# Optimization experiments

Measured on AMD Instinct MI355X. Metric: run time of the kernel, lower is better.

Reference implementation:

```python
import jax, jax.numpy as jnp
import numpy as np

K = 1  # top-k experts per image


def cv_squared(v):
    # squared coefficient of variation; torch .var() is unbiased -> ddof=1
    eps = 1e-10
    m = v.mean()
    var = v.var(ddof=1)
    return jnp.where(jnp.abs(m) < eps, jnp.zeros((), v.dtype), var / (m * m + eps))


def setup_inputs() -> dict:
    key = jax.random.key(0)
    k0, k1, k2, k3 = jax.random.split(key, 4)
    B, H, W, C, E, HID = 64, 32, 32, 512, 5, 2048
    x = jax.random.normal(k0, (B, H, W, C), jnp.float32)
    # xavier-uniform-like scale for the gate
    gate_scale = float(np.sqrt(6.0 / (C + E)))
    w_gate = jax.random.uniform(k1, (C, E), jnp.float32, -gate_scale, gate_scale)
    W1 = jax.random.normal(k2, (E, C, HID), jnp.float32) * 0.02
    b1 = jnp.zeros((E, HID), jnp.float32)
    W2 = jax.random.normal(k3, (E, HID, C), jnp.float32) * 0.02
    b2 = jnp.zeros((E, C), jnp.float32)
    return {"x": x, "w_gate": w_gate, "W1": W1, "b1": b1, "W2": W2, "b2": b2}


def reference(x, w_gate, W1, b1, W2, b2):
    B, H, W_, C = x.shape
    E = w_gate.shape[1]
    xt = x.reshape(B, H * W_, C)              # [B, T, C] tokens
    xg = x.mean(axis=(1, 2))                  # [B, C] per-image gating feature

    # eval-mode noisy_top_k_gating (no noise): clean logits, clamp, top-k softmax
    logits = jnp.clip(xg @ w_gate, -50.0, 50.0)          # [B, E]
    top_logits, top_idx = jax.lax.top_k(logits, min(K + 1, E))
    tk_logits = top_logits[:, :K]
    tk_idx = top_idx[:, :K]                               # [B, K]
    tk_gates = jax.nn.softmax(tk_logits, axis=1)          # [B, K]
    gates = jnp.zeros_like(logits).at[jnp.arange(B)[:, None], tk_idx].set(tk_gates)

    importance = gates.sum(axis=0)                        # [E]
    load = (gates > 0).sum(axis=0).astype(jnp.float32)    # [E]
    loss = jnp.clip(cv_squared(importance) + cv_squared(load), 0.0, 1000.0)

    # dispatch: every token of image b goes through its top-K experts
    y = jnp.zeros_like(xt)
    for ki in range(K):
        idx = tk_idx[:, ki]                               # [B] expert id per image
        h = jnp.einsum('btd,bdh->bth', xt, W1[idx]) + b1[idx][:, None, :]
        h = jax.nn.gelu(h, approximate=False)             # torch nn.GELU default (erf)
        o = jnp.einsum('bth,bhd->btd', h, W2[idx]) + b2[idx][:, None, :]
        y = y + tk_gates[:, ki][:, None, None] * o

    return y.reshape(B, H, W_, C), loss
```

## Files before the change

### kernel.cpp

```cpp
#include <hip/hip_runtime.h>
#include <hip/hip_bf16.h>
#include <math.h>

typedef __attribute__((ext_vector_type(4))) float f4_t;
typedef __attribute__((ext_vector_type(8))) short s8_t;

constexpr int Bc = 64;
constexpr int Tc = 1024;
constexpr int Cc = 512;
constexpr int Ec = 5;
constexpr int HIDc = 2048;

__device__ __forceinline__ void async_copy16(const void* gsrc, void* ldst) {
  __builtin_amdgcn_global_load_lds(
      (const __attribute__((address_space(1))) unsigned int*)gsrc,
      (__attribute__((address_space(3))) unsigned int*)ldst, 16, 0, 0);
}

__device__ __forceinline__ float gelu_f(float v) {
  float u = v * 0.70710678118654752f;
  float ax = fabsf(u);
  float t = __frcp_rn(1.0f + 0.3275911f * ax);
  float p = t * (0.254829592f +
           t * (-0.284496736f +
           t * (1.421413741f +
           t * (-1.453152027f +
           t * 1.061405429f))));
  float er = 1.0f - p * __expf(-u * u);
  er = copysignf(er, u);
  return 0.5f * v * (1.0f + er);
}


__global__ void k_prep(const float* __restrict__ x, ushort* __restrict__ xbf,
                       float* __restrict__ part) {
  int b = blockIdx.x, p = blockIdx.y, tid = threadIdx.x;
  const float4* xp = (const float4*)(x + ((size_t)b * Tc + (size_t)p * 128) * Cc);
  ushort4* op = (ushort4*)(xbf + ((size_t)b * Tc + (size_t)p * 128) * Cc);
  int c4 = tid & 127, r0 = tid >> 7;
  float4 s = {0.f, 0.f, 0.f, 0.f};
  for (int r = r0; r < 128; r += 2) {
    float4 v = xp[(size_t)r * 128 + c4];
    s.x += v.x; s.y += v.y; s.z += v.z; s.w += v.w;
    union { __hip_bfloat16 h[4]; ushort4 u; } cv;
    cv.h[0] = __float2bfloat16(v.x);
    cv.h[1] = __float2bfloat16(v.y);
    cv.h[2] = __float2bfloat16(v.z);
    cv.h[3] = __float2bfloat16(v.w);
    op[(size_t)r * 128 + c4] = cv.u;
  }
  __shared__ float4 sh[128];
  if (r0) sh[c4] = s;
  __syncthreads();
  if (!r0) {
    float4 o = sh[c4];
    s.x += o.x; s.y += o.y; s.z += o.z; s.w += o.w;
    ((float4*)part)[(size_t)(b * 8 + p) * 128 + c4] = s;
  }
}

__global__ void k_partial(const float* __restrict__ x, float* __restrict__ part) {
  int b = blockIdx.x, p = blockIdx.y, tid = threadIdx.x;
  const float* xp = x + ((size_t)b * Tc + (size_t)p * 128) * Cc;
  float s0 = 0.f, s1 = 0.f;
  for (int t = 0; t < 128; ++t) {
    s0 += xp[(size_t)t * Cc + tid];
    s1 += xp[(size_t)t * Cc + tid + 256];
  }
  part[(size_t)(b * 8 + p) * Cc + tid] = s0;
  part[(size_t)(b * 8 + p) * Cc + tid + 256] = s1;
}

__global__ void k_cvt_x(const float* __restrict__ src, ushort* __restrict__ dst, int n4) {
  int i = blockIdx.x * blockDim.x + threadIdx.x;
  int stride = gridDim.x * blockDim.x;
  const float4* s4 = (const float4*)src;
  ushort4* d4 = (ushort4*)dst;
  for (; i < n4; i += stride) {
    float4 v = s4[i];
    union { __hip_bfloat16 h[4]; ushort4 u; } cv;
    cv.h[0] = __float2bfloat16(v.x);
    cv.h[1] = __float2bfloat16(v.y);
    cv.h[2] = __float2bfloat16(v.z);
    cv.h[3] = __float2bfloat16(v.w);
    d4[i] = cv.u;
  }
}

__global__ void k_xg_logits(const float* __restrict__ part, const float* __restrict__ wg,
                            float* __restrict__ logits) {
  __shared__ float xg[Cc];
  __shared__ float red[Ec][4];
  int b = blockIdx.x, tid = threadIdx.x;
  for (int c = tid; c < Cc; c += 256) {
    float s = 0.f;
#pragma unroll
    for (int p = 0; p < 8; ++p) s += part[(size_t)(b * 8 + p) * Cc + c];
    xg[c] = s * (1.0f / 1024.0f);
  }
  __syncthreads();
  float le[Ec] = {0.f, 0.f, 0.f, 0.f, 0.f};
  for (int c = tid; c < Cc; c += 256) {
    float v = xg[c];
#pragma unroll
    for (int e = 0; e < Ec; ++e) le[e] += v * wg[c * Ec + e];
  }
#pragma unroll
  for (int e = 0; e < Ec; ++e) {
    float v = le[e];
#pragma unroll
    for (int off = 32; off > 0; off >>= 1) v += __shfl_down(v, off);
    if ((tid & 63) == 0) red[e][tid >> 6] = v;
  }
  __syncthreads();
  if (tid < Ec) {
    float v = red[tid][0] + red[tid][1] + red[tid][2] + red[tid][3];
    v = fminf(fmaxf(v, -50.f), 50.f);
    logits[b * Ec + tid] = v;
  }
}

__global__ void k_gate(const float* __restrict__ logits, int* __restrict__ idx,
                       float* __restrict__ loss_out) {
  __shared__ int cnt[Ec];
  int tid = threadIdx.x;
  if (tid < Ec) cnt[tid] = 0;
  __syncthreads();
  if (tid < Bc) {
    const float* lb = logits + tid * Ec;
    int best = 0;
    float bv = lb[0];
#pragma unroll
    for (int e = 1; e < Ec; ++e) {
      float v = lb[e];
      if (v > bv) { bv = v; best = e; }
    }
    idx[tid] = best;
    atomicAdd(&cnt[best], 1);
  }
  __syncthreads();
  if (tid == 0) {
    const float mean = (float)Bc / (float)Ec;
    float var = 0.f;
#pragma unroll
    for (int e = 0; e < Ec; ++e) {
      float d = (float)cnt[e] - mean;
      var += d * d;
    }
    var *= (1.0f / (Ec - 1));
    float loss = 2.f * (var / (mean * mean + 1e-10f));
    loss = fminf(fmaxf(loss, 0.f), 1000.f);
    *loss_out = loss;
  }
}

__global__ void k_transpose_cvt(const float* __restrict__ src, __hip_bfloat16* __restrict__ dst,
                                int K, int N) {
  __shared__ float tile[32][33];
  int e = blockIdx.z;
  int kb = blockIdx.y * 32, nb = blockIdx.x * 32;
  const float* s = src + (size_t)e * K * N;
  __hip_bfloat16* d = dst + (size_t)e * K * N;
  int lx = threadIdx.x & 31, ly = threadIdx.x >> 5;
#pragma unroll
  for (int r = 0; r < 4; ++r) {
    int k = kb + ly + r * 8;
    tile[ly + r * 8][lx] = s[(size_t)k * N + nb + lx];
  }
  __syncthreads();
#pragma unroll
  for (int r = 0; r < 4; ++r) {
    int n = nb + ly + r * 8;
    d[(size_t)n * K + kb + lx] = __float2bfloat16(tile[lx][ly + r * 8]);
  }
}


__global__ __launch_bounds__(256, 2) void k_gemm1(
    const __hip_bfloat16* __restrict__ xbf, const __hip_bfloat16* __restrict__ w1t,
    const float* __restrict__ b1, const int* __restrict__ idx, int b0, int nz,
    __hip_bfloat16* __restrict__ h) {
  constexpr int K = Cc;
  constexpr int N = HIDc;
  constexpr int NT = K / 64;
  constexpr int NBX = N / 128, NBY = Tc / 128;
  __shared__ short lds[2][2][128 * 64];

  int nwg = NBX * NBY * nz;
  int cpx = nwg >> 3;
  int lg = (blockIdx.x & 7) * cpx + (blockIdx.x >> 3);
  int bx = lg % NBX, by = (lg / NBX) % NBY, bz = lg / (NBX * NBY);

  int e = idx[b0 + bz];
  int m0 = by * 128, n0 = bx * 128;
  const short* Ab = (const short*)xbf + ((size_t)bz * Tc + m0) * K;
  const short* Bb = (const short*)w1t + ((size_t)e * N + n0) * K;
  int tid = threadIdx.x, l = tid & 63, w = tid >> 6;
  int wr = w >> 1, wc = w & 1;

  const short* gA[4];
  const short* gB[4];
  int loff[4];
#pragma unroll
  for (int i = 0; i < 4; ++i) {
    int sp = i * 256 + tid;
    int r = sp >> 3;
    int c8 = ((sp & 7) ^ (r & 7)) << 3;
    gA[i] = Ab + (size_t)r * K + c8;
    gB[i] = Bb + (size_t)r * K + c8;
    loff[i] = sp * 16;
  }

  int arow = wr * 64 + (l & 15);
  int brow = wc * 64 + (l & 15);
  int s0 = (((l >> 4)) ^ (l & 7)) << 4;
  int s1 = (((l >> 4) + 4) ^ (l & 7)) << 4;

  f4_t acc[4][4] = {};

#pragma unroll
  for (int i = 0; i < 4; ++i) {
    async_copy16(gA[i], (char*)&lds[0][0][0] + loff[i]);
    async_copy16(gB[i], (char*)&lds[0][1][0] + loff[i]);
  }
  __syncthreads();

  for (int t = 0; t < NT; ++t) {
    int cur = t & 1;
    if (t + 1 < NT) {
      int k0 = (t + 1) * 64;
#pragma unroll
      for (int i = 0; i < 4; ++i) {
        async_copy16(gA[i] + k0, (char*)&lds[cur ^ 1][0][0] + loff[i]);
        async_copy16(gB[i] + k0, (char*)&lds[cur ^ 1][1][0] + loff[i]);
      }
    }
    const char* As = (const char*)&lds[cur][0][0];
    const char* Bs = (const char*)&lds[cur][1][0];
#pragma unroll
    for (int kk = 0; kk < 2; ++kk) {
      int sk = kk ? s1 : s0;
      s8_t a[4], b[4];
#pragma unroll
      for (int f = 0; f < 4; ++f) a[f] = *(const s8_t*)(As + (arow + f * 16) * 128 + sk);
#pragma unroll
      for (int f = 0; f < 4; ++f) b[f] = *(const s8_t*)(Bs + (brow + f * 16) * 128 + sk);
#pragma unroll
      for (int fm = 0; fm < 4; ++fm)
#pragma unroll
        for (int fn = 0; fn < 4; ++fn)
          acc[fm][fn] = __builtin_amdgcn_mfma_f32_16x16x32_bf16(a[fm], b[fn], acc[fm][fn], 0, 0, 0);
    }
    __syncthreads();
  }

  short* chunk = &lds[0][0][0] + w * (64 * 80);
  const float* bias = b1 + (size_t)e * N;
#pragma unroll
  for (int fn = 0; fn < 4; ++fn) {
    float bv = bias[n0 + wc * 64 + fn * 16 + (l & 15)];
#pragma unroll
    for (int fm = 0; fm < 4; ++fm) {
      int r4 = fm * 16 + ((l >> 4) << 2);
#pragma unroll
      for (int j = 0; j < 4; ++j) {
        float v = gelu_f(acc[fm][fn][j] + bv);
        chunk[(r4 + j) * 80 + fn * 16 + (l & 15)] =
            (short)__bfloat16_as_ushort(__float2bfloat16(v));
      }
    }
  }
  short* hb = (short*)(h + (size_t)bz * Tc * N);
  int cc = (l & 7) * 8;
#pragma unroll
  for (int p = 0; p < 8; ++p) {
    int rr = p * 8 + (l >> 3);
    s8_t v = *(const s8_t*)(chunk + rr * 80 + cc);
    *(s8_t*)(hb + (size_t)(m0 + wr * 64 + rr) * N + n0 + wc * 64 + cc) = v;
  }
}

__global__ __launch_bounds__(512, 2) void k_gemm2(
    const __hip_bfloat16* __restrict__ h, const __hip_bfloat16* __restrict__ w2t,
    const float* __restrict__ b2, const int* __restrict__ idx, int b0, int nz,
    float* __restrict__ out) {
  constexpr int K = HIDc;
  constexpr int N = Cc;
  constexpr int NT = K / 64;
  constexpr int NBX = N / 256, NBY = Tc / 256;
  __shared__ short lds[2][2][256 * 64];

  int nwg = NBX * NBY * nz;
  int cpx = nwg >> 3;
  int lg = (blockIdx.x & 7) * cpx + (blockIdx.x >> 3);
  int bx = lg % NBX, by = (lg / NBX) % NBY, bz = lg / (NBX * NBY);

  int e = idx[b0 + bz];
  int m0 = by * 256, n0 = bx * 256;
  const short* Ab = (const short*)h + ((size_t)bz * Tc + m0) * K;
  const short* Bb = (const short*)w2t + ((size_t)e * N + n0) * K;
  int tid = threadIdx.x, l = tid & 63, w = tid >> 6;
  int wr = w >> 2, wc = w & 3;

  const short* gA[4];
  const short* gB[4];
  int loff[4];
#pragma unroll
  for (int i = 0; i < 4; ++i) {
    int sp = i * 512 + tid;
    int r = sp >> 3;
    int c8 = ((sp & 7) ^ (r & 7)) << 3;
    gA[i] = Ab + (size_t)r * K + c8;
    gB[i] = Bb + (size_t)r * K + c8;
    loff[i] = sp * 16;
  }

  int arow = wr * 128 + (l & 15);
  int brow = wc * 64 + (l & 15);
  int s0 = (((l >> 4)) ^ (l & 7)) << 4;
  int s1 = (((l >> 4) + 4) ^ (l & 7)) << 4;

  f4_t acc[8][4] = {};

#pragma unroll
  for (int i = 0; i < 4; ++i) {
    async_copy16(gA[i], (char*)&lds[0][0][0] + loff[i]);
    async_copy16(gB[i], (char*)&lds[0][1][0] + loff[i]);
  }
  __syncthreads();

  for (int t = 0; t < NT; ++t) {
    int cur = t & 1;
    if (t + 1 < NT) {
      int k0 = (t + 1) * 64;
#pragma unroll
      for (int i = 0; i < 4; ++i) {
        async_copy16(gA[i] + k0, (char*)&lds[cur ^ 1][0][0] + loff[i]);
        async_copy16(gB[i] + k0, (char*)&lds[cur ^ 1][1][0] + loff[i]);
      }
    }
    const char* As = (const char*)&lds[cur][0][0];
    const char* Bs = (const char*)&lds[cur][1][0];
#pragma unroll
    for (int kk = 0; kk < 2; ++kk) {
      int sk = kk ? s1 : s0;
      s8_t a[8], b[4];
#pragma unroll
      for (int f = 0; f < 8; ++f) a[f] = *(const s8_t*)(As + (arow + f * 16) * 128 + sk);
#pragma unroll
      for (int f = 0; f < 4; ++f) b[f] = *(const s8_t*)(Bs + (brow + f * 16) * 128 + sk);
#pragma unroll
      for (int fm = 0; fm < 8; ++fm)
#pragma unroll
        for (int fn = 0; fn < 4; ++fn)
          acc[fm][fn] = __builtin_amdgcn_mfma_f32_16x16x32_bf16(a[fm], b[fn], acc[fm][fn], 0, 0, 0);
    }
    __syncthreads();
  }

  float* ob = out + (size_t)(b0 + bz) * Tc * N;
  const float* bias = b2 + (size_t)e * N;
#pragma unroll
  for (int fn = 0; fn < 4; ++fn) {
    int col = n0 + wc * 64 + fn * 16 + (l & 15);
    float bv = bias[col];
#pragma unroll
    for (int fm = 0; fm < 8; ++fm) {
      int rbase = m0 + wr * 128 + fm * 16 + ((l >> 4) << 2);
#pragma unroll
      for (int j = 0; j < 4; ++j) {
        ob[(size_t)(rbase + j) * N + col] = acc[fm][fn][j] + bv;
      }
    }
  }
}

extern "C" void kernel_launch(void* const* d_in, const int* in_sizes, int n_in,
                              void* d_out, int out_size, void* d_ws, size_t ws_size,
                              hipStream_t stream) {
  const float* x  = (const float*)d_in[0];
  const float* wg = (const float*)d_in[1];
  const float* W1 = (const float*)d_in[2];
  const float* b1 = (const float*)d_in[3];
  const float* W2 = (const float*)d_in[4];
  const float* b2 = (const float*)d_in[5];
  float* out = (float*)d_out;

  char* ws = (char*)d_ws;
  size_t off = 0;
  float* part = (float*)(ws + off); off += (size_t)Bc * 8 * Cc * 4;
  float* logits = (float*)(ws + off); off += (size_t)Bc * Ec * 4;
  int* idx = (int*)(ws + off); off += (size_t)Bc * 4;
  off = (off + 255) & ~(size_t)255;
  __hip_bfloat16* w1t = (__hip_bfloat16*)(ws + off); off += (size_t)Ec * HIDc * Cc * 2;
  __hip_bfloat16* w2t = (__hip_bfloat16*)(ws + off); off += (size_t)Ec * HIDc * Cc * 2;
  size_t dynoff = (off + 255) & ~(size_t)255;

  const size_t x_all = (size_t)Bc * Tc * Cc * 2;
  const size_t x_per_b = (size_t)Tc * Cc * 2;
  const size_t h_per_b = (size_t)Tc * HIDc * 2;

  k_transpose_cvt<<<dim3(HIDc / 32, Cc / 32, Ec), 256, 0, stream>>>(W1, w1t, Cc, HIDc);
  k_transpose_cvt<<<dim3(Cc / 32, HIDc / 32, Ec), 256, 0, stream>>>(W2, w2t, HIDc, Cc);

  if (ws_size >= dynoff + x_all + h_per_b) {
    __hip_bfloat16* xbf = (__hip_bfloat16*)(ws + dynoff);
    __hip_bfloat16* hbf = (__hip_bfloat16*)(ws + dynoff + x_all);
    int cb = (int)((ws_size - dynoff - x_all) / h_per_b);
    if (cb > Bc) cb = Bc;

    k_prep<<<dim3(Bc, 8), 256, 0, stream>>>(x, (ushort*)xbf, part);
    k_xg_logits<<<dim3(Bc), 256, 0, stream>>>(part, wg, logits);
    k_gate<<<dim3(1), 256, 0, stream>>>(logits, idx, out + ((size_t)out_size - 1));

    for (int b0 = 0; b0 < Bc; b0 += cb) {
      int c = (Bc - b0) < cb ? (Bc - b0) : cb;
      const __hip_bfloat16* xc = xbf + (size_t)b0 * Tc * Cc;
      k_gemm1<<<dim3((HIDc / 128) * (Tc / 128) * c), 256, 0, stream>>>(
          xc, w1t, b1, idx, b0, c, hbf);
      k_gemm2<<<dim3((Cc / 256) * (Tc / 256) * c), 512, 0, stream>>>(
          hbf, w2t, b2, idx, b0, c, out);
    }
  } else {
    size_t avail = ws_size > dynoff ? ws_size - dynoff : 0;
    int cb = (int)(avail / (x_per_b + h_per_b));
    if (cb > Bc) cb = Bc;
    if (cb < 1) cb = 1;
    __hip_bfloat16* xbf = (__hip_bfloat16*)(ws + dynoff);
    __hip_bfloat16* hbf = (__hip_bfloat16*)(ws + dynoff + (size_t)cb * x_per_b);

    k_partial<<<dim3(Bc, 8), 256, 0, stream>>>(x, part);
    k_xg_logits<<<dim3(Bc), 256, 0, stream>>>(part, wg, logits);
    k_gate<<<dim3(1), 256, 0, stream>>>(logits, idx, out + ((size_t)out_size - 1));

    for (int b0 = 0; b0 < Bc; b0 += cb) {
      int c = (Bc - b0) < cb ? (Bc - b0) : cb;
      int n4 = c * (Tc * Cc / 4);
      k_cvt_x<<<dim3(1024), 256, 0, stream>>>(x + (size_t)b0 * Tc * Cc, (ushort*)xbf, n4);
      k_gemm1<<<dim3((HIDc / 128) * (Tc / 128) * c), 256, 0, stream>>>(
          xbf, w1t, b1, idx, 0 + b0, c, hbf);
      k_gemm2<<<dim3((Cc / 256) * (Tc / 256) * c), 512, 0, stream>>>(
          hbf, w2t, b2, idx, b0, c, out);
    }
  }
}
```

Measured before the change: 495.1 us.

## Enlarge GEMM1 tiles to 256x256 and share a pipelined K-loop with MFMA priority

GEMM1 moves from 128x128 tiles with 256 threads to 256x256 tiles with 512 threads, matching GEMM2 and raising data reuse per block. Both GEMMs now run a common macro K-loop that issues the next stage's async LDS loads before waiting with a partial vmcnt, replaces __syncthreads with raw barriers, and raises wave priority around the MFMA section. GEMM1's epilogue writes GELU output through LDS in two halves. In exchange, GEMM1 uses more LDS and registers per block, launches fewer blocks, and relies on hand-placed waitcnt/barrier ordering being correct.

Measured after the change: 484.4 us. 1.02x faster.

```diff
diff --git a/kernel.cpp b/kernel.cpp
--- a/kernel.cpp
+++ b/kernel.cpp
@@ -176,15 +176,89 @@
 }
 
 
-__global__ __launch_bounds__(256, 2) void k_gemm1(
+#define GEMM_PRELUDE(KDIM)                                               \
+  int tid = threadIdx.x, l = tid & 63, w = tid >> 6;                     \
+  int wr = w >> 2, wc = w & 3;                                           \
+  const short* gA[4];                                                    \
+  const short* gB[4];                                                    \
+  int loff[4];                                                           \
+  _Pragma("unroll")                                                      \
+  for (int i = 0; i < 4; ++i) {                                          \
+    int sp = i * 512 + tid;                                              \
+    int r = sp >> 3;                                                     \
+    int c8 = ((sp & 7) ^ (r & 7)) << 3;                                  \
+    gA[i] = Ab + (size_t)r * (KDIM) + c8;                                \
+    gB[i] = Bb + (size_t)r * (KDIM) + c8;                                \
+    loff[i] = sp * 16;                                                   \
+  }                                                                      \
+  int abase = (wr * 128 + (l & 15)) * 128;                               \
+  int bbase = (wc * 64 + (l & 15)) * 128;                                \
+  int s0 = (((l >> 4)) ^ (l & 7)) << 4;                                  \
+  int s1 = (((l >> 4) + 4) ^ (l & 7)) << 4;
+
+#define STAGE(bi, kt)                                                    \
+  {                                                                      \
+    int k0_ = (kt) * 64;                                                 \
+    char* da_ = (char*)&lds[bi][0][0];                                   \
+    char* db_ = (char*)&lds[bi][1][0];                                   \
+    _Pragma("unroll")                                                    \
+    for (int i = 0; i < 4; ++i) {                                        \
+      async_copy16(gA[i] + k0_, da_ + loff[i]);                          \
+      async_copy16(gB[i] + k0_, db_ + loff[i]);                          \
+    }                                                                    \
+  }
+
+#define COMPUTE(bi)                                                      \
+  {                                                                      \
+    const char* As_ = (const char*)&lds[bi][0][0];                       \
+    const char* Bs_ = (const char*)&lds[bi][1][0];                       \
+    __builtin_amdgcn_s_setprio(1);                                       \
+    _Pragma("unroll")                                                    \
+    for (int kk = 0; kk < 2; ++kk) {                                     \
+      int sk = kk ? s1 : s0;                                             \
+      s8_t a[8], b[4];                                                   \
+      _Pragma("unroll")                                                  \
+      for (int f = 0; f < 8; ++f)                                        \
+        a[f] = *(const s8_t*)(As_ + abase + f * 2048 + sk);              \
+      _Pragma("unroll")                                                  \
+      for (int f = 0; f < 4; ++f)                                        \
+        b[f] = *(const s8_t*)(Bs_ + bbase + f * 2048 + sk);              \
+      _Pragma("unroll")                                                  \
+      for (int fm = 0; fm < 8; ++fm)                                     \
+        _Pragma("unroll")                                                \
+        for (int fn = 0; fn < 4; ++fn)                                   \
+          acc[fm][fn] =                                                  \
+              __builtin_amdgcn_mfma_f32_16x16x32_bf16(a[fm], b[fn],      \
+                                                      acc[fm][fn], 0, 0, 0); \
+    }                                                                    \
+    __builtin_amdgcn_s_setprio(0);                                       \
+  }
+
+#define KLOOP(NT)                                                        \
+  STAGE(0, 0);                                                           \
+  for (int t = 0; t < (NT) - 1; ++t) {                                   \
+    STAGE((t + 1) & 1, t + 1);                                           \
+    asm volatile("s_waitcnt vmcnt(8)" ::: "memory");                     \
+    __builtin_amdgcn_s_barrier();                                        \
+    asm volatile("" ::: "memory");                                       \
+    COMPUTE(t & 1);                                                      \
+    __builtin_amdgcn_s_barrier();                                        \
+    asm volatile("" ::: "memory");                                       \
+  }                                                                      \
+  asm volatile("s_waitcnt vmcnt(0)" ::: "memory");                       \
+  __builtin_amdgcn_s_barrier();                                          \
+  asm volatile("" ::: "memory");                                         \
+  COMPUTE(((NT) - 1) & 1);
+
+__global__ __launch_bounds__(512, 2) void k_gemm1(
     const __hip_bfloat16* __restrict__ xbf, const __hip_bfloat16* __restrict__ w1t,
     const float* __restrict__ b1, const int* __restrict__ idx, int b0, int nz,
     __hip_bfloat16* __restrict__ h) {
   constexpr int K = Cc;
   constexpr int N = HIDc;
   constexpr int NT = K / 64;
-  constexpr int NBX = N / 128, NBY = Tc / 128;
-  __shared__ short lds[2][2][128 * 64];
+  constexpr int NBX = N / 256, NBY = Tc / 256;
+  __shared__ short lds[2][2][256 * 64];
 
   int nwg = NBX * NBY * nz;
   int cpx = nwg >> 3;
@@ -192,91 +266,42 @@
   int bx = lg % NBX, by = (lg / NBX) % NBY, bz = lg / (NBX * NBY);
 
   int e = idx[b0 + bz];
-  int m0 = by * 128, n0 = bx * 128;
+  int m0 = by * 256, n0 = bx * 256;
   const short* Ab = (const short*)xbf + ((size_t)bz * Tc + m0) * K;
   const short* Bb = (const short*)w1t + ((size_t)e * N + n0) * K;
-  int tid = threadIdx.x, l = tid & 63, w = tid >> 6;
-  int wr = w >> 1, wc = w & 1;
-
-  const short* gA[4];
-  const short* gB[4];
-  int loff[4];
-#pragma unroll
-  for (int i = 0; i < 4; ++i) {
-    int sp = i * 256 + tid;
-    int r = sp >> 3;
-    int c8 = ((sp & 7) ^ (r & 7)) << 3;
-    gA[i] = Ab + (size_t)r * K + c8;
-    gB[i] = Bb + (size_t)r * K + c8;
-    loff[i] = sp * 16;
-  }
-
-  int arow = wr * 64 + (l & 15);
-  int brow = wc * 64 + (l & 15);
-  int s0 = (((l >> 4)) ^ (l & 7)) << 4;
-  int s1 = (((l >> 4) + 4) ^ (l & 7)) << 4;
-
-  f4_t acc[4][4] = {};
-
-#pragma unroll
-  for (int i = 0; i < 4; ++i) {
-    async_copy16(gA[i], (char*)&lds[0][0][0] + loff[i]);
-    async_copy16(gB[i], (char*)&lds[0][1][0] + loff[i]);
-  }
-  __syncthreads();
-
-  for (int t = 0; t < NT; ++t) {
-    int cur = t & 1;
-    if (t + 1 < NT) {
-      int k0 = (t + 1) * 64;
-#pragma unroll
-      for (int i = 0; i < 4; ++i) {
-        async_copy16(gA[i] + k0, (char*)&lds[cur ^ 1][0][0] + loff[i]);
-        async_copy16(gB[i] + k0, (char*)&lds[cur ^ 1][1][0] + loff[i]);
+
+  GEMM_PRELUDE(K)
+  f4_t acc[8][4] = {};
+  KLOOP(NT)
+
+  __syncthreads();
+  short* chunk = &lds[0][0][0] + w * (64 * 72);
+  const float* bias = b1 + (size_t)e * N;
+  short* hb = (short*)(h + (size_t)bz * Tc * N);
+  int cc2 = (l & 7) * 8;
+#pragma unroll
+  for (int p = 0; p < 2; ++p) {
+#pragma unroll
+    for (int fn = 0; fn < 4; ++fn) {
+      float bv = bias[n0 + wc * 64 + fn * 16 + (l & 15)];
+#pragma unroll
+      for (int fm = 0; fm < 4; ++fm) {
+        int rl = fm * 16 + ((l >> 4) << 2);
+#pragma unroll
+        for (int j = 0; j < 4; ++j) {
+          float v = gelu_f(acc[p * 4 + fm][fn][j] + bv);
+          chunk[(rl + j) * 72 + fn * 16 + (l & 15)] =
+              (short)__bfloat16_as_ushort(__float2bfloat16(v));
+        }
       }
     }
-    const char* As = (const char*)&lds[cur][0][0];
-    const char* Bs = (const char*)&lds[cur][1][0];
-#pragma unroll
-    for (int kk = 0; kk < 2; ++kk) {
-      int sk = kk ? s1 : s0;
-      s8_t a[4], b[4];
-#pragma unroll
-      for (int f = 0; f < 4; ++f) a[f] = *(const s8_t*)(As + (arow + f * 16) * 128 + sk);
-#pragma unroll
-      for (int f = 0; f < 4; ++f) b[f] = *(const s8_t*)(Bs + (brow + f * 16) * 128 + sk);
-#pragma unroll
-      for (int fm = 0; fm < 4; ++fm)
-#pragma unroll
-        for (int fn = 0; fn < 4; ++fn)
-          acc[fm][fn] = __builtin_amdgcn_mfma_f32_16x16x32_bf16(a[fm], b[fn], acc[fm][fn], 0, 0, 0);
-    }
-    __syncthreads();
-  }
-
-  short* chunk = &lds[0][0][0] + w * (64 * 80);
-  const float* bias = b1 + (size_t)e * N;
-#pragma unroll
-  for (int fn = 0; fn < 4; ++fn) {
-    float bv = bias[n0 + wc * 64 + fn * 16 + (l & 15)];
-#pragma unroll
-    for (int fm = 0; fm < 4; ++fm) {
-      int r4 = fm * 16 + ((l >> 4) << 2);
-#pragma unroll
-      for (int j = 0; j < 4; ++j) {
-        float v = gelu_f(acc[fm][fn][j] + bv);
-        chunk[(r4 + j) * 80 + fn * 16 + (l & 15)] =
-            (short)__bfloat16_as_ushort(__float2bfloat16(v));
-      }
-    }
-  }
-  short* hb = (short*)(h + (size_t)bz * Tc * N);
-  int cc = (l & 7) * 8;
-#pragma unroll
-  for (int p = 0; p < 8; ++p) {
-    int rr = p * 8 + (l >> 3);
-    s8_t v = *(const s8_t*)(chunk + rr * 80 + cc);
-    *(s8_t*)(hb + (size_t)(m0 + wr * 64 + rr) * N + n0 + wc * 64 + cc) = v;
+#pragma unroll
+    for (int q = 0; q < 8; ++q) {
+      int rr = q * 8 + (l >> 3);
+      s8_t v = *(const s8_t*)(chunk + rr * 72 + cc2);
+      *(s8_t*)(hb + (size_t)(m0 + wr * 128 + p * 64 + rr) * N + n0 + wc * 64 + cc2) = v;
+    }
+    asm volatile("s_waitcnt lgkmcnt(0)" ::: "memory");
   }
 }
 
@@ -299,64 +324,10 @@
   int m0 = by * 256, n0 = bx * 256;
   const short* Ab = (const short*)h + ((size_t)bz * Tc + m0) * K;
   const short* Bb = (const short*)w2t + ((size_t)e * N + n0) * K;
-  int tid = threadIdx.x, l = tid & 63, w = tid >> 6;
-  int wr = w >> 2, wc = w & 3;
-
-  const short* gA[4];
-  const short* gB[4];
-  int loff[4];
-#pragma unroll
-  for (int i = 0; i < 4; ++i) {
-    int sp = i * 512 + tid;
-    int r = sp >> 3;
-    int c8 = ((sp & 7) ^ (r & 7)) << 3;
-    gA[i] = Ab + (size_t)r * K + c8;
-    gB[i] = Bb + (size_t)r * K + c8;
-    loff[i] = sp * 16;
-  }
-
-  int arow = wr * 128 + (l & 15);
-  int brow = wc * 64 + (l & 15);
-  int s0 = (((l >> 4)) ^ (l & 7)) << 4;
-  int s1 = (((l >> 4) + 4) ^ (l & 7)) << 4;
-
+
+  GEMM_PRELUDE(K)
   f4_t acc[8][4] = {};
-
-#pragma unroll
-  for (int i = 0; i < 4; ++i) {
-    async_copy16(gA[i], (char*)&lds[0][0][0] + loff[i]);
-    async_copy16(gB[i], (char*)&lds[0][1][0] + loff[i]);
-  }
-  __syncthreads();
-
-  for (int t = 0; t < NT; ++t) {
-    int cur = t & 1;
-    if (t + 1 < NT) {
-      int k0 = (t + 1) * 64;
-#pragma unroll
-      for (int i = 0; i < 4; ++i) {
-        async_copy16(gA[i] + k0, (char*)&lds[cur ^ 1][0][0] + loff[i]);
-        async_copy16(gB[i] + k0, (char*)&lds[cur ^ 1][1][0] + loff[i]);
-      }
-    }
-    const char* As = (const char*)&lds[cur][0][0];
-    const char* Bs = (const char*)&lds[cur][1][0];
-#pragma unroll
-    for (int kk = 0; kk < 2; ++kk) {
-      int sk = kk ? s1 : s0;
-      s8_t a[8], b[4];
-#pragma unroll
-      for (int f = 0; f < 8; ++f) a[f] = *(const s8_t*)(As + (arow + f * 16) * 128 + sk);
-#pragma unroll
-      for (int f = 0; f < 4; ++f) b[f] = *(const s8_t*)(Bs + (brow + f * 16) * 128 + sk);
-#pragma unroll
-      for (int fm = 0; fm < 8; ++fm)
-#pragma unroll
-        for (int fn = 0; fn < 4; ++fn)
-          acc[fm][fn] = __builtin_amdgcn_mfma_f32_16x16x32_bf16(a[fm], b[fn], acc[fm][fn], 0, 0, 0);
-    }
-    __syncthreads();
-  }
+  KLOOP(NT)
 
   float* ob = out + (size_t)(b0 + bz) * Tc * N;
   const float* bias = b2 + (size_t)e * N;
@@ -416,7 +387,7 @@
     for (int b0 = 0; b0 < Bc; b0 += cb) {
       int c = (Bc - b0) < cb ? (Bc - b0) : cb;
       const __hip_bfloat16* xc = xbf + (size_t)b0 * Tc * Cc;
-      k_gemm1<<<dim3((HIDc / 128) * (Tc / 128) * c), 256, 0, stream>>>(
+      k_gemm1<<<dim3((HIDc / 256) * (Tc / 256) * c), 512, 0, stream>>>(
           xc, w1t, b1, idx, b0, c, hbf);
       k_gemm2<<<dim3((Cc / 256) * (Tc / 256) * c), 512, 0, stream>>>(
           hbf, w2t, b2, idx, b0, c, out);
@@ -437,8 +408,8 @@
       int c = (Bc - b0) < cb ? (Bc - b0) : cb;
       int n4 = c * (Tc * Cc / 4);
       k_cvt_x<<<dim3(1024), 256, 0, stream>>>(x + (size_t)b0 * Tc * Cc, (ushort*)xbf, n4);
-      k_gemm1<<<dim3((HIDc / 128) * (Tc / 128) * c), 256, 0, stream>>>(
-          xbf, w1t, b1, idx, 0 + b0, c, hbf);
+      k_gemm1<<<dim3((HIDc / 256) * (Tc / 256) * c), 512, 0, stream>>>(
+          xbf, w1t, b1, idx, b0, c, hbf);
       k_gemm2<<<dim3((Cc / 256) * (Tc / 256) * c), 512, 0, stream>>>(
           hbf, w2t, b2, idx, b0, c, out);
     }
```
